# Kernel optimization log

Measured on AMD Instinct MI355X. Metric: run time of the kernel, lower is better.

## Reference

```python
import jax, jax.numpy as jnp
import numpy as np

S = 256
H = 4       # n_heads
DH = 32     # head_dim
D = H * DH  # model dim
EPS = 1e-5


def setup_inputs() -> dict:
    key = jax.random.key(0)
    ks = jax.random.split(key, 12)
    x = jax.random.normal(ks[0], (1, S, S, D), dtype=jnp.float32)
    # attention mask: mostly 0, occasionally large negative (masked)
    keep = jax.random.uniform(ks[1], (1, 1, S, S)) < 0.9
    attn_mask = jnp.where(keep, 0.0, -1e9).astype(jnp.float32)
    sc = 1.0 / np.sqrt(D)
    ln_w = jnp.ones((D,), jnp.float32)
    ln_b = jnp.zeros((D,), jnp.float32)
    Wb = jax.random.normal(ks[2], (H, D), jnp.float32) * sc   # bias projection (linear.weight)
    Wq = jax.random.normal(ks[3], (D, D), jnp.float32) * sc
    Wk = jax.random.normal(ks[4], (D, D), jnp.float32) * sc
    Wv = jax.random.normal(ks[5], (D, D), jnp.float32) * sc
    Wg = jax.random.normal(ks[6], (D, D), jnp.float32) * sc
    Wo = jax.random.normal(ks[7], (D, D), jnp.float32) * sc
    return {"x": x, "attn_mask": attn_mask, "ln_w": ln_w, "ln_b": ln_b,
            "Wb": Wb, "Wq": Wq, "Wk": Wk, "Wv": Wv, "Wg": Wg, "Wo": Wo}


def reference(x, attn_mask, ln_w, ln_b, Wb, Wq, Wk, Wv, Wg, Wo):
    # x: [1,S,S,D] pair representation; ending=False so no transpose of S axes.
    x0 = x[0]  # [S,S,D]
    mu = jnp.mean(x0, axis=-1, keepdims=True)
    var = jnp.mean(jnp.square(x0 - mu), axis=-1, keepdims=True)
    xn = (x0 - mu) * jax.lax.rsqrt(var + EPS) * ln_w + ln_b  # [S,S,D]

    # triangle bias: [S,S,H] -> [1,H,S,S] (broadcast over batch-of-rows)
    bias = jnp.einsum('bqd,hd->hbq', xn, Wb)[None]  # [1,H,S,S]

    def heads(W):
        return jnp.einsum('bqd,ed->bqe', xn, W).reshape(S, S, H, DH).transpose(0, 2, 1, 3)

    q, k, v = heads(Wq), heads(Wk), heads(Wv)  # each [S,H,S,DH]

    scale = 1.0 / np.sqrt(DH)
    scores = jnp.einsum('bhqd,bhkd->bhqk', q, k) * scale + bias + attn_mask  # [S,H,S,S]
    attn = jax.nn.softmax(scores, axis=-1)
    o = jnp.einsum('bhqk,bhkd->bhqd', attn, v)  # [S,H,S,DH]
    o = o.transpose(0, 2, 1, 3).reshape(S, S, D)

    g = jnp.einsum('bqd,ed->bqe', xn, Wg)
    out = jnp.einsum('bqe,fe->bqf', o * jax.nn.sigmoid(g), Wo)  # [S,S,D]
    return out[None]  # [1,S,S,D]
```

## Files before the change

kernel.cpp:

```cpp
#include <hip/hip_runtime.h>
#include <hip/hip_bf16.h>

#define S_DIM 256
#define D_DIM 128
#define H_DIM 4
#define NPOS  (S_DIM * S_DIM)

typedef __attribute__((ext_vector_type(8))) short  short8;
typedef __attribute__((ext_vector_type(4))) float  f32x4;

__device__ __forceinline__ float b2f(unsigned short u) {
    union { float f; unsigned int u32; } c; c.u32 = ((unsigned int)u) << 16; return c.f;
}
__device__ __forceinline__ unsigned short f2b(float f) {
    __hip_bfloat16 h = __float2bfloat16(f);
    return *reinterpret_cast<unsigned short*>(&h);
}

__global__ __launch_bounds__(256) void ln_biasmask_kernel(
    const float* __restrict__ x, const float* __restrict__ mask,
    const float* __restrict__ lnw, const float* __restrict__ lnb,
    const float* __restrict__ Wb, float* __restrict__ bm)
{
    const int wave = threadIdx.x >> 6, lane = threadIdx.x & 63;
    const int p = blockIdx.x * 4 + wave;

    float2 v = ((const float2*)x)[p * 64 + lane];
    float s = v.x + v.y, ss = v.x * v.x + v.y * v.y;
    #pragma unroll
    for (int m = 1; m < 64; m <<= 1) { s += __shfl_xor(s, m); ss += __shfl_xor(ss, m); }
    float mean = s * (1.f / 128.f);
    float var  = ss * (1.f / 128.f) - mean * mean;
    float rstd = rsqrtf(var + 1e-5f);

    float xn0 = (v.x - mean) * rstd * lnw[lane * 2]     + lnb[lane * 2];
    float xn1 = (v.y - mean) * rstd * lnw[lane * 2 + 1] + lnb[lane * 2 + 1];

    float mval = mask[p];
    #pragma unroll
    for (int h = 0; h < H_DIM; h++) {
        float d = xn0 * Wb[h * 128 + lane * 2] + xn1 * Wb[h * 128 + lane * 2 + 1];
        #pragma unroll
        for (int m = 1; m < 64; m <<= 1) d += __shfl_xor(d, m);
        if (lane == 0) bm[(long)h * NPOS + p] = d + mval;
    }
}

__global__ __launch_bounds__(256) void proj_ln_kernel(
    const float* __restrict__ x,
    const float* __restrict__ lnw, const float* __restrict__ lnb,
    const float* __restrict__ Wq, const float* __restrict__ Wk,
    const float* __restrict__ Wv, const float* __restrict__ Wg,
    int p0, unsigned short* __restrict__ strip)
{
    __shared__ __align__(16) unsigned short A_lds[64 * 136];
    __shared__ __align__(16) unsigned short W_lds[128 * 136];
    const int tid = threadIdx.x;
    const int m0 = blockIdx.x * 64;
    const int gy = blockIdx.y;
    const float* W = (gy == 0) ? Wq : (gy == 1) ? Wk : (gy == 2) ? Wv : Wg;

    const int lr = tid >> 4, c8 = (tid & 15) * 8;
    #pragma unroll
    for (int i = 0; i < 4; i++) {
        int row = lr + i * 16;
        const float* src = x + (size_t)(p0 + m0 + row) * 128 + c8;
        float4 f0 = *(const float4*)(src);
        float4 f1 = *(const float4*)(src + 4);
        float s  = f0.x + f0.y + f0.z + f0.w + f1.x + f1.y + f1.z + f1.w;
        float ss = f0.x*f0.x + f0.y*f0.y + f0.z*f0.z + f0.w*f0.w
                 + f1.x*f1.x + f1.y*f1.y + f1.z*f1.z + f1.w*f1.w;
        #pragma unroll
        for (int m = 1; m < 16; m <<= 1) { s += __shfl_xor(s, m); ss += __shfl_xor(ss, m); }
        float mean = s * (1.f / 128.f);
        float var  = ss * (1.f / 128.f) - mean * mean;
        float rstd = rsqrtf(var + 1e-5f);
        float xv[8] = {f0.x, f0.y, f0.z, f0.w, f1.x, f1.y, f1.z, f1.w};
        unsigned short pk[8];
        #pragma unroll
        for (int j = 0; j < 8; j++)
            pk[j] = f2b((xv[j] - mean) * rstd * lnw[c8 + j] + lnb[c8 + j]);
        *(uint4*)(&A_lds[row * 136 + c8]) = *(const uint4*)pk;
    }
    #pragma unroll
    for (int i = 0; i < 8; i++) {
        int wr = lr + i * 16;
        const float* src = W + (size_t)wr * 128 + c8;
        float4 f0 = *(const float4*)(src);
        float4 f1 = *(const float4*)(src + 4);
        unsigned short pk[8] = {f2b(f0.x), f2b(f0.y), f2b(f0.z), f2b(f0.w),
                                f2b(f1.x), f2b(f1.y), f2b(f1.z), f2b(f1.w)};
        *(uint4*)(&W_lds[wr * 136 + c8]) = *(const uint4*)pk;
    }
    __syncthreads();

    const int w = tid >> 6, lane = tid & 63;
    const int l16 = lane & 15, quad = lane >> 4;
    f32x4 acc[8];
    #pragma unroll
    for (int nt = 0; nt < 8; nt++) acc[nt] = (f32x4){0.f, 0.f, 0.f, 0.f};

    #pragma unroll
    for (int k0 = 0; k0 < 128; k0 += 32) {
        short8 a = *(const short8*)(&A_lds[(w * 16 + l16) * 136 + k0 + quad * 8]);
        #pragma unroll
        for (int nt = 0; nt < 8; nt++) {
            short8 b = *(const short8*)(&W_lds[(nt * 16 + l16) * 136 + k0 + quad * 8]);
            acc[nt] = __builtin_amdgcn_mfma_f32_16x16x32_bf16(a, b, acc[nt], 0, 0, 0);
        }
    }

    #pragma unroll
    for (int nt = 0; nt < 8; nt++)
        #pragma unroll
        for (int rr = 0; rr < 4; rr++) {
            int row = m0 + w * 16 + quad * 4 + rr;
            strip[(size_t)row * 512 + gy * 128 + nt * 16 + l16] = f2b(acc[nt][rr]);
        }
}

__global__ __launch_bounds__(256) void attn_kernel(
    const unsigned short* __restrict__ strip, const float* __restrict__ bm,
    int b0, float* __restrict__ out)
{
    __shared__ __align__(16) unsigned short VT_lds[32 * 264];
    __shared__ __align__(16) unsigned short P_lds[4 * 16 * 264];
    const int bl = blockIdx.x, h = blockIdx.y;
    const int b  = b0 + bl;
    const int tid = threadIdx.x;

    {
        const int row = tid >> 2, chunk = (tid & 3) * 8;
        #pragma unroll
        for (int i = 0; i < 4; i++) {
            int rr = row + i * 64;
            uint4 v = *(const uint4*)(strip + (size_t)(bl * 256 + rr) * 512 + 256 + h * 32 + chunk);
            unsigned short vs[8] = {
                (unsigned short)(v.x & 0xffff), (unsigned short)(v.x >> 16),
                (unsigned short)(v.y & 0xffff), (unsigned short)(v.y >> 16),
                (unsigned short)(v.z & 0xffff), (unsigned short)(v.z >> 16),
                (unsigned short)(v.w & 0xffff), (unsigned short)(v.w >> 16)};
            #pragma unroll
            for (int j = 0; j < 8; j++) VT_lds[(chunk + j) * 264 + rr] = vs[j];
        }
    }
    __syncthreads();

    const int w = tid >> 6, lane = tid & 63;
    const int l16 = lane & 15, quad = lane >> 4;
    const float* bmh = bm + (long)h * NPOS;
    unsigned short* P_w = P_lds + w * 16 * 264;
    const float scale = 0.17677669529663687f;

    #pragma unroll 1
    for (int i = 0; i < 4; i++) {
        const int q0 = (w * 4 + i) * 16;
        short8 aq = *(const short8*)(strip + (size_t)(bl * 256 + q0 + l16) * 512 + h * 32 + quad * 8);

        float sc[16][4];
        #pragma unroll
        for (int nt = 0; nt < 16; nt++) {
            short8 kb = *(const short8*)(strip + (size_t)(bl * 256 + nt * 16 + l16) * 512 + 128 + h * 32 + quad * 8);
            f32x4 c = (f32x4){0.f, 0.f, 0.f, 0.f};
            c = __builtin_amdgcn_mfma_f32_16x16x32_bf16(aq, kb, c, 0, 0, 0);
            #pragma unroll
            for (int rr = 0; rr < 4; rr++) {
                int row = q0 + quad * 4 + rr;
                sc[nt][rr] = c[rr] * scale + bmh[(long)row * 256 + nt * 16 + l16];
            }
        }
        float rsum[4];
        #pragma unroll
        for (int rr = 0; rr < 4; rr++) {
            float m = sc[0][rr];
            #pragma unroll
            for (int nt = 1; nt < 16; nt++) m = fmaxf(m, sc[nt][rr]);
            #pragma unroll
            for (int msk = 1; msk < 16; msk <<= 1) m = fmaxf(m, __shfl_xor(m, msk));
            float ssum = 0.f;
            #pragma unroll
            for (int nt = 0; nt < 16; nt++) {
                float pv = __expf(sc[nt][rr] - m);
                sc[nt][rr] = pv; ssum += pv;
            }
            #pragma unroll
            for (int msk = 1; msk < 16; msk <<= 1) ssum += __shfl_xor(ssum, msk);
            rsum[rr] = ssum;
        }
        #pragma unroll
        for (int nt = 0; nt < 16; nt++)
            #pragma unroll
            for (int rr = 0; rr < 4; rr++)
                P_w[(quad * 4 + rr) * 264 + nt * 16 + l16] = f2b(sc[nt][rr]);

        f32x4 oacc[2];
        oacc[0] = (f32x4){0.f, 0.f, 0.f, 0.f};
        oacc[1] = (f32x4){0.f, 0.f, 0.f, 0.f};
        #pragma unroll
        for (int kt = 0; kt < 8; kt++) {
            short8 pa = *(const short8*)(&P_w[l16 * 264 + kt * 32 + quad * 8]);
            #pragma unroll
            for (int nh = 0; nh < 2; nh++) {
                short8 vb = *(const short8*)(&VT_lds[(nh * 16 + l16) * 264 + kt * 32 + quad * 8]);
                oacc[nh] = __builtin_amdgcn_mfma_f32_16x16x32_bf16(pa, vb, oacc[nh], 0, 0, 0);
            }
        }
        #pragma unroll
        for (int rr = 0; rr < 4; rr++) {
            int row = q0 + quad * 4 + rr;
            float inv = 1.f / rsum[rr];
            #pragma unroll
            for (int nh = 0; nh < 2; nh++) {
                int cl = nh * 16 + l16;
                float g = b2f(strip[(size_t)(bl * 256 + row) * 512 + 384 + h * 32 + cl]);
                float ov = oacc[nh][rr] * inv;
                ov = ov / (1.f + __expf(-g));
                out[((long)b * 256 + row) * 128 + h * 32 + cl] = ov;
            }
        }
    }
}

__global__ __launch_bounds__(256) void outproj_mfma_kernel(
    const float* __restrict__ Wo, float* out)
{
    __shared__ __align__(16) unsigned short A_lds[64 * 136];
    __shared__ __align__(16) unsigned short W_lds[128 * 136];
    const int tid = threadIdx.x;
    const int m0 = blockIdx.x * 64;

    const int lr = tid >> 4, c8 = (tid & 15) * 8;
    #pragma unroll
    for (int i = 0; i < 4; i++) {
        const float* src = out + (size_t)(m0 + lr + i * 16) * 128 + c8;
        float4 f0 = *(const float4*)(src);
        float4 f1 = *(const float4*)(src + 4);
        unsigned short pk[8] = {f2b(f0.x), f2b(f0.y), f2b(f0.z), f2b(f0.w),
                                f2b(f1.x), f2b(f1.y), f2b(f1.z), f2b(f1.w)};
        *(uint4*)(&A_lds[(lr + i * 16) * 136 + c8]) = *(const uint4*)pk;
    }
    #pragma unroll
    for (int i = 0; i < 8; i++) {
        const float* src = Wo + (size_t)(lr + i * 16) * 128 + c8;
        float4 f0 = *(const float4*)(src);
        float4 f1 = *(const float4*)(src + 4);
        unsigned short pk[8] = {f2b(f0.x), f2b(f0.y), f2b(f0.z), f2b(f0.w),
                                f2b(f1.x), f2b(f1.y), f2b(f1.z), f2b(f1.w)};
        *(uint4*)(&W_lds[(lr + i * 16) * 136 + c8]) = *(const uint4*)pk;
    }
    __syncthreads();

    const int w = tid >> 6, lane = tid & 63;
    const int l16 = lane & 15, quad = lane >> 4;
    f32x4 acc[8];
    #pragma unroll
    for (int nt = 0; nt < 8; nt++) acc[nt] = (f32x4){0.f, 0.f, 0.f, 0.f};

    #pragma unroll
    for (int k0 = 0; k0 < 128; k0 += 32) {
        short8 a = *(const short8*)(&A_lds[(w * 16 + l16) * 136 + k0 + quad * 8]);
        #pragma unroll
        for (int nt = 0; nt < 8; nt++) {
            short8 b = *(const short8*)(&W_lds[(nt * 16 + l16) * 136 + k0 + quad * 8]);
            acc[nt] = __builtin_amdgcn_mfma_f32_16x16x32_bf16(a, b, acc[nt], 0, 0, 0);
        }
    }

    #pragma unroll
    for (int nt = 0; nt < 8; nt++)
        #pragma unroll
        for (int rr = 0; rr < 4; rr++) {
            int row = m0 + w * 16 + quad * 4 + rr;
            out[(size_t)row * 128 + nt * 16 + l16] = acc[nt][rr];
        }
}

extern "C" void kernel_launch(void* const* d_in, const int* in_sizes, int n_in,
                              void* d_out, int out_size, void* d_ws, size_t ws_size,
                              hipStream_t stream)
{
    (void)in_sizes; (void)n_in; (void)out_size;
    const float* x    = (const float*)d_in[0];
    const float* mask = (const float*)d_in[1];
    const float* lnw  = (const float*)d_in[2];
    const float* lnb  = (const float*)d_in[3];
    const float* Wb   = (const float*)d_in[4];
    const float* Wq   = (const float*)d_in[5];
    const float* Wk   = (const float*)d_in[6];
    const float* Wv   = (const float*)d_in[7];
    const float* Wg   = (const float*)d_in[8];
    const float* Wo   = (const float*)d_in[9];
    float* out = (float*)d_out;

    const size_t bmB = (size_t)H_DIM * NPOS * sizeof(float);
    int HB = 256;
    while (HB > 16 && bmB + (size_t)HB * 256 * 512 * 2 > ws_size) HB >>= 1;

    char* ws = (char*)d_ws;
    float*          bm    = (float*)ws;
    unsigned short* strip = (unsigned short*)(ws + bmB);

    ln_biasmask_kernel<<<NPOS / 4, 256, 0, stream>>>(x, mask, lnw, lnb, Wb, bm);
    for (int b0 = 0; b0 < S_DIM; b0 += HB) {
        proj_ln_kernel<<<dim3(HB * 4, 4), 256, 0, stream>>>(
            x, lnw, lnb, Wq, Wk, Wv, Wg, b0 * 256, strip);
        attn_kernel<<<dim3(HB, H_DIM), 256, 0, stream>>>(strip, bm, b0, out);
    }
    outproj_mfma_kernel<<<NPOS / 64, 256, 0, stream>>>(Wo, out);
}
```

Baseline: 231.1 us.

## Transpose MFMA outputs for vector stores, split attention over queries, bf16 gated buffer

Swaps the MFMA operand order so each lane holds four consecutive columns of one row, which lets the projection, score-bias and output-projection paths use vectorized loads and stores instead of scattered scalar ones. The attention grid gains a third dimension of size two, so each block handles half the query tiles, and the softmax reductions become per-lane with only two cross-lane shuffles. The gated attention output is now written as bf16 to a separate workspace buffer, so the output projection reads it directly instead of reading fp32 and converting. The cost is more workspace and the K/V tile being loaded twice per head-row, once per z-block.

```diff
diff --git a/kernel.cpp b/kernel.cpp
--- a/kernel.cpp
+++ b/kernel.cpp
@@ -106,26 +106,27 @@
         #pragma unroll
         for (int nt = 0; nt < 8; nt++) {
             short8 b = *(const short8*)(&W_lds[(nt * 16 + l16) * 136 + k0 + quad * 8]);
-            acc[nt] = __builtin_amdgcn_mfma_f32_16x16x32_bf16(a, b, acc[nt], 0, 0, 0);
-        }
-    }
-
-    #pragma unroll
-    for (int nt = 0; nt < 8; nt++)
-        #pragma unroll
-        for (int rr = 0; rr < 4; rr++) {
-            int row = m0 + w * 16 + quad * 4 + rr;
-            strip[(size_t)row * 512 + gy * 128 + nt * 16 + l16] = f2b(acc[nt][rr]);
-        }
+            acc[nt] = __builtin_amdgcn_mfma_f32_16x16x32_bf16(b, a, acc[nt], 0, 0, 0);
+        }
+    }
+
+    const size_t rowbase = (size_t)(m0 + w * 16 + l16) * 512 + gy * 128;
+    #pragma unroll
+    for (int nt = 0; nt < 8; nt++) {
+        uint2 pk;
+        pk.x = (unsigned)f2b(acc[nt][0]) | ((unsigned)f2b(acc[nt][1]) << 16);
+        pk.y = (unsigned)f2b(acc[nt][2]) | ((unsigned)f2b(acc[nt][3]) << 16);
+        *(uint2*)(&strip[rowbase + nt * 16 + quad * 4]) = pk;
+    }
 }
 
 __global__ __launch_bounds__(256) void attn_kernel(
     const unsigned short* __restrict__ strip, const float* __restrict__ bm,
-    int b0, float* __restrict__ out)
+    int b0, unsigned short* __restrict__ gated)
 {
     __shared__ __align__(16) unsigned short VT_lds[32 * 264];
     __shared__ __align__(16) unsigned short P_lds[4 * 16 * 264];
-    const int bl = blockIdx.x, h = blockIdx.y;
+    const int bl = blockIdx.x, h = blockIdx.y, z = blockIdx.z;
     const int b  = b0 + bl;
     const int tid = threadIdx.x;
 
@@ -153,45 +154,54 @@
     const float scale = 0.17677669529663687f;
 
     #pragma unroll 1
-    for (int i = 0; i < 4; i++) {
-        const int q0 = (w * 4 + i) * 16;
-        short8 aq = *(const short8*)(strip + (size_t)(bl * 256 + q0 + l16) * 512 + h * 32 + quad * 8);
+    for (int i = 0; i < 2; i++) {
+        const int q0 = (w * 4 + z * 2 + i) * 16;
+        short8 bq = *(const short8*)(strip + (size_t)(bl * 256 + q0 + l16) * 512 + h * 32 + quad * 8);
+        const float* brow = bmh + (size_t)(q0 + l16) * 256 + quad * 4;
 
         float sc[16][4];
         #pragma unroll
         for (int nt = 0; nt < 16; nt++) {
-            short8 kb = *(const short8*)(strip + (size_t)(bl * 256 + nt * 16 + l16) * 512 + 128 + h * 32 + quad * 8);
+            short8 ka = *(const short8*)(strip + (size_t)(bl * 256 + nt * 16 + l16) * 512 + 128 + h * 32 + quad * 8);
             f32x4 c = (f32x4){0.f, 0.f, 0.f, 0.f};
-            c = __builtin_amdgcn_mfma_f32_16x16x32_bf16(aq, kb, c, 0, 0, 0);
-            #pragma unroll
-            for (int rr = 0; rr < 4; rr++) {
-                int row = q0 + quad * 4 + rr;
-                sc[nt][rr] = c[rr] * scale + bmh[(long)row * 256 + nt * 16 + l16];
-            }
-        }
-        float rsum[4];
-        #pragma unroll
-        for (int rr = 0; rr < 4; rr++) {
-            float m = sc[0][rr];
-            #pragma unroll
-            for (int nt = 1; nt < 16; nt++) m = fmaxf(m, sc[nt][rr]);
-            #pragma unroll
-            for (int msk = 1; msk < 16; msk <<= 1) m = fmaxf(m, __shfl_xor(m, msk));
-            float ssum = 0.f;
-            #pragma unroll
-            for (int nt = 0; nt < 16; nt++) {
-                float pv = __expf(sc[nt][rr] - m);
-                sc[nt][rr] = pv; ssum += pv;
-            }
-            #pragma unroll
-            for (int msk = 1; msk < 16; msk <<= 1) ssum += __shfl_xor(ssum, msk);
-            rsum[rr] = ssum;
-        }
-        #pragma unroll
-        for (int nt = 0; nt < 16; nt++)
-            #pragma unroll
-            for (int rr = 0; rr < 4; rr++)
-                P_w[(quad * 4 + rr) * 264 + nt * 16 + l16] = f2b(sc[nt][rr]);
+            c = __builtin_amdgcn_mfma_f32_16x16x32_bf16(ka, bq, c, 0, 0, 0);
+            float4 bb = *(const float4*)(brow + nt * 16);
+            sc[nt][0] = c[0] * scale + bb.x;
+            sc[nt][1] = c[1] * scale + bb.y;
+            sc[nt][2] = c[2] * scale + bb.z;
+            sc[nt][3] = c[3] * scale + bb.w;
+        }
+
+        float m0 = sc[0][0], m1 = sc[0][1], m2 = sc[0][2], m3 = sc[0][3];
+        #pragma unroll
+        for (int nt = 1; nt < 16; nt++) {
+            m0 = fmaxf(m0, sc[nt][0]); m1 = fmaxf(m1, sc[nt][1]);
+            m2 = fmaxf(m2, sc[nt][2]); m3 = fmaxf(m3, sc[nt][3]);
+        }
+        float m = fmaxf(fmaxf(m0, m1), fmaxf(m2, m3));
+        m = fmaxf(m, __shfl_xor(m, 16));
+        m = fmaxf(m, __shfl_xor(m, 32));
+
+        float s0 = 0.f, s1 = 0.f, s2 = 0.f, s3 = 0.f;
+        #pragma unroll
+        for (int nt = 0; nt < 16; nt++) {
+            float p0_ = __expf(sc[nt][0] - m); sc[nt][0] = p0_; s0 += p0_;
+            float p1_ = __expf(sc[nt][1] - m); sc[nt][1] = p1_; s1 += p1_;
+            float p2_ = __expf(sc[nt][2] - m); sc[nt][2] = p2_; s2 += p2_;
+            float p3_ = __expf(sc[nt][3] - m); sc[nt][3] = p3_; s3 += p3_;
+        }
+        float ssum = (s0 + s1) + (s2 + s3);
+        ssum += __shfl_xor(ssum, 16);
+        ssum += __shfl_xor(ssum, 32);
+        float inv = 1.f / ssum;
+
+        #pragma unroll
+        for (int nt = 0; nt < 16; nt++) {
+            uint2 pk;
+            pk.x = (unsigned)f2b(sc[nt][0]) | ((unsigned)f2b(sc[nt][1]) << 16);
+            pk.y = (unsigned)f2b(sc[nt][2]) | ((unsigned)f2b(sc[nt][3]) << 16);
+            *(uint2*)(&P_w[l16 * 264 + nt * 16 + quad * 4]) = pk;
+        }
 
         f32x4 oacc[2];
         oacc[0] = (f32x4){0.f, 0.f, 0.f, 0.f};
@@ -207,22 +217,23 @@
         }
         #pragma unroll
         for (int rr = 0; rr < 4; rr++) {
+            float invr = __shfl(inv, quad * 4 + rr);
             int row = q0 + quad * 4 + rr;
-            float inv = 1.f / rsum[rr];
             #pragma unroll
             for (int nh = 0; nh < 2; nh++) {
                 int cl = nh * 16 + l16;
                 float g = b2f(strip[(size_t)(bl * 256 + row) * 512 + 384 + h * 32 + cl]);
-                float ov = oacc[nh][rr] * inv;
+                float ov = oacc[nh][rr] * invr;
                 ov = ov / (1.f + __expf(-g));
-                out[((long)b * 256 + row) * 128 + h * 32 + cl] = ov;
+                gated[((size_t)b * 256 + row) * 128 + h * 32 + cl] = f2b(ov);
             }
         }
     }
 }
 
 __global__ __launch_bounds__(256) void outproj_mfma_kernel(
-    const float* __restrict__ Wo, float* out)
+    const unsigned short* __restrict__ gated, const float* __restrict__ Wo,
+    float* __restrict__ out)
 {
     __shared__ __align__(16) unsigned short A_lds[64 * 136];
     __shared__ __align__(16) unsigned short W_lds[128 * 136];
@@ -232,12 +243,9 @@
     const int lr = tid >> 4, c8 = (tid & 15) * 8;
     #pragma unroll
     for (int i = 0; i < 4; i++) {
-        const float* src = out + (size_t)(m0 + lr + i * 16) * 128 + c8;
-        float4 f0 = *(const float4*)(src);
-        float4 f1 = *(const float4*)(src + 4);
-        unsigned short pk[8] = {f2b(f0.x), f2b(f0.y), f2b(f0.z), f2b(f0.w),
-                                f2b(f1.x), f2b(f1.y), f2b(f1.z), f2b(f1.w)};
-        *(uint4*)(&A_lds[(lr + i * 16) * 136 + c8]) = *(const uint4*)pk;
+        int row = lr + i * 16;
+        *(uint4*)(&A_lds[row * 136 + c8]) =
+            *(const uint4*)(gated + (size_t)(m0 + row) * 128 + c8);
     }
     #pragma unroll
     for (int i = 0; i < 8; i++) {
@@ -262,17 +270,14 @@
         #pragma unroll
         for (int nt = 0; nt < 8; nt++) {
             short8 b = *(const short8*)(&W_lds[(nt * 16 + l16) * 136 + k0 + quad * 8]);
-            acc[nt] = __builtin_amdgcn_mfma_f32_16x16x32_bf16(a, b, acc[nt], 0, 0, 0);
-        }
-    }
-
+            acc[nt] = __builtin_amdgcn_mfma_f32_16x16x32_bf16(b, a, acc[nt], 0, 0, 0);
+        }
+    }
+
+    float* orow = out + (size_t)(m0 + w * 16 + l16) * 128;
     #pragma unroll
     for (int nt = 0; nt < 8; nt++)
-        #pragma unroll
-        for (int rr = 0; rr < 4; rr++) {
-            int row = m0 + w * 16 + quad * 4 + rr;
-            out[(size_t)row * 128 + nt * 16 + l16] = acc[nt][rr];
-        }
+        *(f32x4*)(&orow[nt * 16 + quad * 4]) = acc[nt];
 }
 
 extern "C" void kernel_launch(void* const* d_in, const int* in_sizes, int n_in,
@@ -293,18 +298,20 @@
     float* out = (float*)d_out;
 
     const size_t bmB = (size_t)H_DIM * NPOS * sizeof(float);
+    const size_t gB  = (size_t)NPOS * 128 * sizeof(unsigned short);
     int HB = 256;
-    while (HB > 16 && bmB + (size_t)HB * 256 * 512 * 2 > ws_size) HB >>= 1;
+    while (HB > 16 && bmB + gB + (size_t)HB * 256 * 512 * 2 > ws_size) HB >>= 1;
 
     char* ws = (char*)d_ws;
     float*          bm    = (float*)ws;
-    unsigned short* strip = (unsigned short*)(ws + bmB);
+    unsigned short* gated = (unsigned short*)(ws + bmB);
+    unsigned short* strip = (unsigned short*)(ws + bmB + gB);
 
     ln_biasmask_kernel<<<NPOS / 4, 256, 0, stream>>>(x, mask, lnw, lnb, Wb, bm);
     for (int b0 = 0; b0 < S_DIM; b0 += HB) {
         proj_ln_kernel<<<dim3(HB * 4, 4), 256, 0, stream>>>(
             x, lnw, lnb, Wq, Wk, Wv, Wg, b0 * 256, strip);
-        attn_kernel<<<dim3(HB, H_DIM), 256, 0, stream>>>(strip, bm, b0, out);
-    }
-    outproj_mfma_kernel<<<NPOS / 64, 256, 0, stream>>>(Wo, out);
-}
+        attn_kernel<<<dim3(HB, H_DIM, 2), 256, 0, stream>>>(strip, bm, b0, gated);
+    }
+    outproj_mfma_kernel<<<NPOS / 64, 256, 0, stream>>>(gated, Wo, out);
+}
```

Result: slower. 245.4 us (+6.2%).
